# Kernel optimization log

Hardware: AMD Instinct MI355X
Metric: run time of the kernel (lower is better)

Reference implementation:

```python
import jax, jax.numpy as jnp
import numpy as np
from jax import lax

B, C, H, W = 64, 32, 128, 128
E, K = 4, 2
EPS = 1e-5


def setup_inputs() -> dict:
    key = jax.random.key(0)
    ks = jax.random.split(key, 8)
    x = jax.random.normal(ks[0], (B, C, H, W), dtype=jnp.float32)
    weights = jax.random.uniform(ks[1], (B, K), dtype=jnp.float32)
    indices = jax.random.randint(ks[2], (B, K), 0, E, dtype=jnp.int32)
    # stacked per-expert params: conv kernel [E, Co, Ci, 3, 3], BN affine + running stats
    Wc = jax.random.normal(ks[3], (E, C, C, 3, 3), dtype=jnp.float32) * (1.0 / np.sqrt(C * 9))
    gamma = jnp.ones((E, C), dtype=jnp.float32)
    beta = jnp.zeros((E, C), dtype=jnp.float32)
    mean = jax.random.normal(ks[4], (E, C), dtype=jnp.float32) * 0.1
    var = jax.random.uniform(ks[5], (E, C), dtype=jnp.float32) + 0.5
    return {"x": x, "weights": weights, "indices": indices,
            "Wc": Wc, "gamma": gamma, "beta": beta, "mean": mean, "var": var}


def _expert(x, w, g, b, m, v):
    # Conv2d(k=3, s=1, pad=1, no bias) -> BatchNorm2d (inference stats) -> SiLU
    y = lax.conv_general_dilated(x, w, (1, 1), 'SAME',
                                 dimension_numbers=('NCHW', 'OIHW', 'NCHW'))
    scale = (g / jnp.sqrt(v + EPS))[None, :, None, None]
    shift = (b - m * g / jnp.sqrt(v + EPS))[None, :, None, None]
    y = y * scale + shift
    return y * jax.nn.sigmoid(y)  # SiLU


def reference(x, weights, indices, Wc, gamma, beta, mean, var):
    num_experts = Wc.shape[0]
    # combined routing weight per (expert, sample): sum over top-k slots routed to that expert
    onehot = (indices[None, :, :] == jnp.arange(num_experts, dtype=indices.dtype)[:, None, None])  # [E,B,K]
    wcomb = jnp.sum(weights[None, :, :] * onehot.astype(weights.dtype), axis=-1)  # [E,B]
    out = jnp.zeros_like(x)
    for i in range(num_experts):  # small fixed expert count
        y = _expert(x, Wc[i], gamma[i], beta[i], mean[i], var[i])
        out = out + y * wcomb[i][:, None, None, None]
    return out
```

## Files before the change

kernel.cpp:

```cpp
#include <hip/hip_runtime.h>
#include <math.h>


#define B_ 64
#define C_ 32
#define H_ 128
#define W_ 128
#define E_ 4
#define K_ 2
#define EPS_ 1e-5f
#define HW_ (H_ * W_)
#define HP_ 130
#define WP_ 130

#define AROW_B 592
#define A_LDS_B (C_ * AROW_B)
#define XPAD_BYTES ((size_t)B_ * HP_ * WP_ * C_ * 2)
#define AW_OFF   XPAD_BYTES
#define AW_BYTES ((size_t)E_ * A_LDS_B)
#define SCSH_OFF (AW_OFF + AW_BYTES)
#define WS_NEEDED (SCSH_OFF + (size_t)E_ * C_ * 2 * 4)

#define LDS_AW   0
#define LDS_SCSH (2 * A_LDS_B)
#define LDS_TOT  (LDS_SCSH + 512)

typedef __attribute__((ext_vector_type(4))) float  f32x4;
typedef __attribute__((ext_vector_type(8))) short  bf16x8;
typedef __attribute__((ext_vector_type(8))) unsigned short u16x8;
typedef __attribute__((ext_vector_type(4))) unsigned short u16x4;

__device__ inline unsigned short f2bf(float f) {
  unsigned u = __builtin_bit_cast(unsigned, f);
  return (unsigned short)((u + 0x7fffu + ((u >> 16) & 1u)) >> 16);
}

__device__ inline void gload16(const void* g, const void* l) {
  __builtin_amdgcn_global_load_lds(
      (const __attribute__((address_space(1))) unsigned int*)g,
      (__attribute__((address_space(3))) unsigned int*)l, 16, 0, 0);
}

__global__ __launch_bounds__(256, 4)
void prep_kernel(const float* __restrict__ x,
                 const float* __restrict__ Wc,
                 const float* __restrict__ gamma,
                 const float* __restrict__ beta,
                 const float* __restrict__ mean,
                 const float* __restrict__ var,
                 unsigned short* __restrict__ wsu) {
  const int bid = blockIdx.x;
  const int tid = threadIdx.x;

  if (bid >= B_ * HP_) {
    int e = bid - B_ * HP_;
    unsigned short* aw = (unsigned short*)((char*)wsu + AW_OFF) + (size_t)e * (A_LDS_B / 2);
    int co  = tid >> 3;
    int ci4 = (tid & 7) * 4;
    const float* wp = Wc + (((size_t)e * C_ + co) * C_ + ci4) * 9;
    float wv[36];
#pragma unroll
    for (int j = 0; j < 36; ++j) wv[j] = wp[j];
    unsigned short* arow = aw + co * (AROW_B / 2) + ci4;
#pragma unroll
    for (int o = 0; o < 9; ++o) {
      u16x4 pk;
#pragma unroll
      for (int q = 0; q < 4; ++q) pk[q] = f2bf(wv[q * 9 + o]);
      *(u16x4*)(arow + o * C_) = pk;
    }
    if (tid < C_) {
      float g  = gamma[e * C_ + tid];
      float bt = beta[e * C_ + tid];
      float mn = mean[e * C_ + tid];
      float vr = var[e * C_ + tid];
      float sc = g * rsqrtf(vr + EPS_);
      float* scsh = (float*)((char*)wsu + SCSH_OFF);
      scsh[(e * C_ + tid) * 2 + 0] = sc;
      scsh[(e * C_ + tid) * 2 + 1] = bt - mn * sc;
    }
    return;
  }

  const int xg = bid >> 3;
  const int u  = bid & 7;
  const int b  = (xg / HP_) * 8 + u;
  const int hp = xg % HP_;
  unsigned short* xrow = wsu + ((size_t)b * HP_ + hp) * WP_ * C_;

  if (hp == 0 || hp == HP_ - 1) {
    u16x8 z = (u16x8)0;
    for (int c = tid; c < WP_ * C_ / 8; c += 256) *(u16x8*)(xrow + c * 8) = z;
    return;
  }

  __shared__ float tile[C_ * W_];
  const int h = hp - 1;
#pragma unroll
  for (int p = 0; p < 4; ++p) {
    int n  = p * 1024 + tid * 4;
    int c  = n >> 7;
    int px = n & 127;
    *(f32x4*)(tile + n) =
        *(const f32x4*)(x + (((size_t)b * C_ + c) * H_ + h) * W_ + px);
  }
  __syncthreads();

  const int px = tid >> 1;
  const int c0 = (tid & 1) * 16;
  u16x8 o0, o1;
#pragma unroll
  for (int j = 0; j < 8; ++j) o0[j] = f2bf(tile[(c0 + j) * W_ + px]);
#pragma unroll
  for (int j = 0; j < 8; ++j) o1[j] = f2bf(tile[(c0 + 8 + j) * W_ + px]);
  unsigned short* dst = xrow + (px + 1) * C_ + c0;
  *(u16x8*)dst = o0;
  *(u16x8*)(dst + 8) = o1;

  if (tid < 4) {
    int pxb = (tid >> 1) ? (WP_ - 1) : 0;
    int hf  = tid & 1;
    u16x8 z = (u16x8)0;
    unsigned short* d2 = xrow + pxb * C_ + hf * 16;
    *(u16x8*)d2 = z;
    *(u16x8*)(d2 + 8) = z;
  }
}

__global__ __launch_bounds__(256, 3)
void conv_kernel(const unsigned short* __restrict__ xpad,
                 const unsigned short* __restrict__ aw_all,
                 const float* __restrict__ scsh_all,
                 const float* __restrict__ weights,
                 const int* __restrict__ indices,
                 float* __restrict__ out) {
  __shared__ __align__(16) unsigned char lds[LDS_TOT];
  const int tid  = threadIdx.x;
  const int lane = tid & 63;
  const int wid  = tid >> 6;

  const int bid  = blockIdx.x;
  const int xcd  = bid & 7;
  const int ii   = bid >> 3;
  const int b    = (ii >> 5) * 8 + xcd;
  const int reg_ = ii & 31;
  const int rowg = reg_ >> 2;
  const int cseg = reg_ & 3;
  const int c0   = cseg * 32;

  const int   e0  = indices[b * K_ + 0];
  const int   e1  = indices[b * K_ + 1];
  const float wk0 = weights[b * K_ + 0];
  const float wk1 = weights[b * K_ + 1];
  const bool  dup = (e0 == e1);
  const float wka = dup ? (wk0 + wk1) : wk0;

  {
    const int nA = (dup ? 1 : 2) * 1184;
    for (int base = wid * 64; base < nA; base += 256) {
      int c = base + lane;
      int e = (c < 1184) ? e0 : e1;
      int r = (c < 1184) ? c : c - 1184;
      const unsigned short* src = aw_all + (size_t)e * (A_LDS_B / 2) + r * 8;
      if (c < nA) gload16(src, lds + LDS_AW + base * 16);
    }
  }
  if (tid < 2 * C_) {
    int s  = tid >> 5;
    int co = tid & 31;
    int e  = s ? e1 : e0;
    float* d = (float*)(lds + LDS_SCSH) + (s * C_ + co) * 2;
    d[0] = scsh_all[(e * C_ + co) * 2 + 0];
    d[1] = scsh_all[(e * C_ + co) * 2 + 1];
  }
  __syncthreads();

  const int lx = lane & 15;
  const int sl = lane >> 4;
  const float* scshl = (const float*)(lds + LDS_SCSH);

#pragma unroll
  for (int t = 0; t < 2; ++t) {
    const int r0 = rowg * 16 + t * 8 + wid * 2;

    const unsigned short* base =
        xpad + ((size_t)(b * HP_ + r0) * WP_ + c0 + lx) * C_ + sl * 8;

    auto loadrow = [&](bf16x8* dst, int hr) {
#pragma unroll
      for (int s = 0; s < 6; ++s)
        dst[s] = *(const bf16x8*)(base + ((size_t)hr * WP_ + (s / 3) * 16 + (s % 3)) * C_);
    };

    f32x4 acc[2][4][2];
#pragma unroll
    for (int s = 0; s < 2; ++s)
#pragma unroll
      for (int mt = 0; mt < 4; ++mt)
#pragma unroll
        for (int nc = 0; nc < 2; ++nc) acc[s][mt][nc] = (f32x4){0.f, 0.f, 0.f, 0.f};

    bf16x8 FA[6], FB[6];
    loadrow(FA, 0);
    loadrow(FB, 1);

#pragma unroll
    for (int dy = 0; dy < 3; ++dy) {
      bf16x8 FC[6];
      if (dy < 2) loadrow(FC, dy + 2);

#pragma unroll
      for (int dx = 0; dx < 3; ++dx) {
        const int o = dy * 3 + dx;
        bf16x8 bf0[2], bf1[2];
#pragma unroll
        for (int nc = 0; nc < 2; ++nc)
          bf0[nc] = *(const bf16x8*)(lds + LDS_AW + (nc * 16 + lx) * AROW_B + o * 64 + sl * 16);
        if (!dup) {
#pragma unroll
          for (int nc = 0; nc < 2; ++nc)
            bf1[nc] = *(const bf16x8*)(lds + LDS_AW + A_LDS_B + (nc * 16 + lx) * AROW_B + o * 64 + sl * 16);
        }
#pragma unroll
        for (int j = 0; j < 2; ++j)
#pragma unroll
          for (int m2 = 0; m2 < 2; ++m2) {
            bf16x8 A = j ? FB[m2 * 3 + dx] : FA[m2 * 3 + dx];
#pragma unroll
            for (int nc = 0; nc < 2; ++nc)
              acc[0][j * 2 + m2][nc] =
                  __builtin_amdgcn_mfma_f32_16x16x32_bf16(A, bf0[nc], acc[0][j * 2 + m2][nc], 0, 0, 0);
            if (!dup) {
#pragma unroll
              for (int nc = 0; nc < 2; ++nc)
                acc[1][j * 2 + m2][nc] =
                    __builtin_amdgcn_mfma_f32_16x16x32_bf16(A, bf1[nc], acc[1][j * 2 + m2][nc], 0, 0, 0);
            }
          }
      }
#pragma unroll
      for (int s = 0; s < 6; ++s) { FA[s] = FB[s]; FB[s] = FC[s]; }
    }

    f32x4 res[4][2];
#pragma unroll
    for (int mt = 0; mt < 4; ++mt)
#pragma unroll
      for (int nc = 0; nc < 2; ++nc) res[mt][nc] = (f32x4){0.f, 0.f, 0.f, 0.f};

#pragma unroll
    for (int s = 0; s < 2; ++s) {
      if (s == 1 && dup) break;
      float wk = s ? wk1 : wka;
#pragma unroll
      for (int nc = 0; nc < 2; ++nc) {
        int co = nc * 16 + lx;
        float sc = scshl[(s * C_ + co) * 2 + 0];
        float sh = scshl[(s * C_ + co) * 2 + 1];
#pragma unroll
        for (int mt = 0; mt < 4; ++mt) {
#pragma unroll
          for (int r = 0; r < 4; ++r) {
            float y = acc[s][mt][nc][r] * sc + sh;
            float sig = 1.f / (1.f + __expf(-y));
            res[mt][nc][r] += wk * y * sig;
          }
        }
      }
    }

#pragma unroll
    for (int j = 0; j < 2; ++j)
#pragma unroll
      for (int m2 = 0; m2 < 2; ++m2)
#pragma unroll
        for (int nc = 0; nc < 2; ++nc) {
          int co = nc * 16 + lx;
          float* ob = out + ((size_t)b * C_ + co) * HW_ +
                      (size_t)(r0 + j) * W_ + c0 + m2 * 16 + sl * 4;
          *(f32x4*)ob = res[j * 2 + m2][nc];
        }
  }
}

#define FHALO 18
#define FNPX (FHALO * FHALO)
#define FPX_B 64
#define FIN_LDS_B (FNPX * FPX_B)
#define FSC_OFF (FIN_LDS_B + 2 * A_LDS_B)
#define FLDS_TOTAL (FSC_OFF + 2 * C_ * 8)
#define TH 16
#define TW 16

__global__ __launch_bounds__(256, 2)
void moe_fallback_kernel(const float* __restrict__ x,
                         const float* __restrict__ weights,
                         const int* __restrict__ indices,
                         const float* __restrict__ Wc,
                         const float* __restrict__ gamma,
                         const float* __restrict__ beta,
                         const float* __restrict__ mean,
                         const float* __restrict__ var,
                         float* __restrict__ out) {
  __shared__ __align__(16) unsigned char lds[FLDS_TOTAL];
  unsigned char* in_t = lds;
  unsigned char* aw0  = lds + FIN_LDS_B;
  unsigned char* aw1  = lds + FIN_LDS_B + A_LDS_B;
  float*         scsh = (float*)(lds + FSC_OFF);

  const int tid = threadIdx.x;
  const int tiles_per_row = W_ / TW;
  const int tiles_per_img = (H_ / TH) * tiles_per_row;
  const int b    = blockIdx.x / tiles_per_img;
  const int tile = blockIdx.x % tiles_per_img;
  const int th0  = (tile / tiles_per_row) * TH;
  const int tw0  = (tile % tiles_per_row) * TW;

  const int   e0  = indices[b * K_ + 0];
  const int   e1  = indices[b * K_ + 1];
  const float wk0 = weights[b * K_ + 0];
  const float wk1 = weights[b * K_ + 1];
  const bool  dup = (e0 == e1);
  const float wka = dup ? (wk0 + wk1) : wk0;

  const float* xb = x + (size_t)b * C_ * HW_;
  for (int i = tid; i < FNPX * 4; i += 256) {
    int px = i % FNPX;
    int cb = i / FNPX;
    int hy = px / FHALO, hx = px % FHALO;
    int gh = th0 + hy - 1, gw = tw0 + hx - 1;
    u16x8 pk = (u16x8)0;
    if (gh >= 0 && gh < H_ && gw >= 0 && gw < W_) {
      const float* src = xb + (size_t)(cb * 8) * HW_ + (size_t)gh * W_ + gw;
#pragma unroll
      for (int j = 0; j < 8; ++j) pk[j] = f2bf(src[(size_t)j * HW_]);
    }
    int slot = cb ^ (px & 3);
    *(u16x8*)(in_t + px * FPX_B + slot * 16) = pk;
  }
  {
    int co  = tid >> 3;
    int ci4 = (tid & 7) * 4;
#pragma unroll
    for (int s = 0; s < 2; ++s) {
      int e = s ? e1 : e0;
      const float* wp = Wc + (size_t)e * C_ * C_ * 9 + (size_t)co * C_ * 9 + (size_t)ci4 * 9;
      float wv[36];
#pragma unroll
      for (int j = 0; j < 36; ++j) wv[j] = wp[j];
      unsigned char* arow = (s ? aw1 : aw0) + co * AROW_B + ci4 * 2;
#pragma unroll
      for (int o = 0; o < 9; ++o) {
        u16x4 pk;
#pragma unroll
        for (int q = 0; q < 4; ++q) pk[q] = f2bf(wv[q * 9 + o]);
        *(u16x4*)(arow + o * 64) = pk;
      }
    }
  }
  if (tid < 64) {
    int s  = tid >> 5;
    int co = tid & 31;
    int e  = s ? e1 : e0;
    float g  = gamma[e * C_ + co];
    float bt = beta[e * C_ + co];
    float mn = mean[e * C_ + co];
    float vr = var[e * C_ + co];
    float sc = g * rsqrtf(vr + EPS_);
    scsh[(s * C_ + co) * 2 + 0] = sc;
    scsh[(s * C_ + co) * 2 + 1] = bt - mn * sc;
  }
  __syncthreads();

  const int lane = tid & 63;
  const int w    = tid >> 6;
  const int lx   = lane & 15;
  const int sl   = lane >> 4;

  f32x4 acc[2][2][4];
#pragma unroll
  for (int s = 0; s < 2; ++s)
#pragma unroll
    for (int m = 0; m < 2; ++m)
#pragma unroll
      for (int j = 0; j < 4; ++j) acc[s][m][j] = (f32x4){0.f, 0.f, 0.f, 0.f};

  int dy = 0, dx = 0;
#pragma unroll 1
  for (int o = 0; o < 9; ++o) {
    bf16x8 bf[4];
#pragma unroll
    for (int j = 0; j < 4; ++j) {
      int hp   = (4 * w + j + dy) * FHALO + (lx + dx);
      int slot = sl ^ (hp & 3);
      bf[j] = *(const bf16x8*)(in_t + hp * FPX_B + slot * 16);
    }
    bf16x8 af0[2], af1[2];
#pragma unroll
    for (int m = 0; m < 2; ++m) {
      int ro = (m * 16 + lx) * AROW_B + o * 64 + sl * 16;
      af0[m] = *(const bf16x8*)(aw0 + ro);
      af1[m] = *(const bf16x8*)(aw1 + ro);
    }
#pragma unroll
    for (int m = 0; m < 2; ++m)
#pragma unroll
      for (int j = 0; j < 4; ++j)
        acc[0][m][j] = __builtin_amdgcn_mfma_f32_16x16x32_bf16(af0[m], bf[j], acc[0][m][j], 0, 0, 0);
    if (!dup) {
#pragma unroll
      for (int m = 0; m < 2; ++m)
#pragma unroll
        for (int j = 0; j < 4; ++j)
          acc[1][m][j] = __builtin_amdgcn_mfma_f32_16x16x32_bf16(af1[m], bf[j], acc[1][m][j], 0, 0, 0);
    }
    if (++dx == 3) { dx = 0; ++dy; }
  }

  float res[2][4][4];
#pragma unroll
  for (int m = 0; m < 2; ++m)
#pragma unroll
    for (int j = 0; j < 4; ++j)
#pragma unroll
      for (int r = 0; r < 4; ++r) res[m][j][r] = 0.f;

#pragma unroll
  for (int s = 0; s < 2; ++s) {
    if (s == 1 && dup) break;
    float wk = s ? wk1 : wka;
#pragma unroll
    for (int m = 0; m < 2; ++m)
#pragma unroll
      for (int r = 0; r < 4; ++r) {
        int co = m * 16 + sl * 4 + r;
        float sc = scsh[(s * C_ + co) * 2 + 0];
        float sh = scsh[(s * C_ + co) * 2 + 1];
#pragma unroll
        for (int j = 0; j < 4; ++j) {
          float y = acc[s][m][j][r] * sc + sh;
          float sig = 1.f / (1.f + __expf(-y));
          res[m][j][r] += wk * y * sig;
        }
      }
  }
#pragma unroll
  for (int m = 0; m < 2; ++m)
#pragma unroll
    for (int r = 0; r < 4; ++r) {
      int co = m * 16 + sl * 4 + r;
      float* ob = out + ((size_t)b * C_ + co) * HW_ + (size_t)th0 * W_ + tw0 + lx;
#pragma unroll
      for (int j = 0; j < 4; ++j)
        ob[(size_t)(4 * w + j) * W_] = res[m][j][r];
    }
}

extern "C" void kernel_launch(void* const* d_in, const int* in_sizes, int n_in,
                              void* d_out, int out_size, void* d_ws, size_t ws_size,
                              hipStream_t stream) {
  const float* x       = (const float*)d_in[0];
  const float* weights = (const float*)d_in[1];
  const int*   indices = (const int*)d_in[2];
  const float* Wc      = (const float*)d_in[3];
  const float* gamma   = (const float*)d_in[4];
  const float* beta    = (const float*)d_in[5];
  const float* mean    = (const float*)d_in[6];
  const float* var     = (const float*)d_in[7];
  float* out = (float*)d_out;

  if (d_ws != nullptr && ws_size >= WS_NEEDED) {
    unsigned short* wsu = (unsigned short*)d_ws;
    const unsigned short* aw_all   = (const unsigned short*)((char*)d_ws + AW_OFF);
    const float*          scsh_all = (const float*)((char*)d_ws + SCSH_OFF);
    prep_kernel<<<B_ * HP_ + E_, 256, 0, stream>>>(x, Wc, gamma, beta, mean, var, wsu);
    conv_kernel<<<2048, 256, 0, stream>>>(wsu, aw_all, scsh_all, weights, indices, out);
  } else {
    moe_fallback_kernel<<<B_ * 64, 256, 0, stream>>>(
        x, weights, indices, Wc, gamma, beta, mean, var, out);
  }
}
```

Measured before the change: 103.7 us.

## Halve conv grid, process 4 row-tiles per block with prefetch and MFMA priority

```diff
diff --git a/kernel.cpp b/kernel.cpp
--- a/kernel.cpp
+++ b/kernel.cpp
@@ -142,8 +142,8 @@
   const int bid  = blockIdx.x;
   const int xcd  = bid & 7;
   const int ii   = bid >> 3;
-  const int b    = (ii >> 5) * 8 + xcd;
-  const int reg_ = ii & 31;
+  const int b    = (ii >> 4) * 8 + xcd;
+  const int reg_ = ii & 15;
   const int rowg = reg_ >> 2;
   const int cseg = reg_ & 3;
   const int c0   = cseg * 32;
@@ -173,24 +173,33 @@
     d[0] = scsh_all[(e * C_ + co) * 2 + 0];
     d[1] = scsh_all[(e * C_ + co) * 2 + 1];
   }
-  __syncthreads();
 
   const int lx = lane & 15;
   const int sl = lane >> 4;
+
+  const unsigned short* cbase =
+      xpad + ((size_t)b * HP_ * WP_ + c0 + lx) * C_ + sl * 8;
+
+#define LOADROW(dst, rbase, hr)                                              \
+  {                                                                          \
+    const unsigned short* _p = cbase + ((size_t)((rbase) + (hr)) * WP_) * C_; \
+    _Pragma("unroll")                                                        \
+    for (int s_ = 0; s_ < 6; ++s_)                                           \
+      dst[s_] = *(const bf16x8*)(_p + ((s_ / 3) * 16 + (s_ % 3)) * C_);      \
+  }
+
+  bf16x8 FA[6], FB[6];
+  const int r0base0 = rowg * 32 + wid * 2;
+  LOADROW(FA, r0base0, 0)
+  LOADROW(FB, r0base0, 1)
+
+  __syncthreads();
+
   const float* scshl = (const float*)(lds + LDS_SCSH);
 
-#pragma unroll
-  for (int t = 0; t < 2; ++t) {
-    const int r0 = rowg * 16 + t * 8 + wid * 2;
-
-    const unsigned short* base =
-        xpad + ((size_t)(b * HP_ + r0) * WP_ + c0 + lx) * C_ + sl * 8;
-
-    auto loadrow = [&](bf16x8* dst, int hr) {
-#pragma unroll
-      for (int s = 0; s < 6; ++s)
-        dst[s] = *(const bf16x8*)(base + ((size_t)hr * WP_ + (s / 3) * 16 + (s % 3)) * C_);
-    };
+#pragma unroll 1
+  for (int t = 0; t < 4; ++t) {
+    const int r0 = rowg * 32 + t * 8 + wid * 2;
 
     f32x4 acc[2][4][2];
 #pragma unroll
@@ -199,15 +208,11 @@
       for (int mt = 0; mt < 4; ++mt)
 #pragma unroll
         for (int nc = 0; nc < 2; ++nc) acc[s][mt][nc] = (f32x4){0.f, 0.f, 0.f, 0.f};
-
-    bf16x8 FA[6], FB[6];
-    loadrow(FA, 0);
-    loadrow(FB, 1);
 
 #pragma unroll
     for (int dy = 0; dy < 3; ++dy) {
       bf16x8 FC[6];
-      if (dy < 2) loadrow(FC, dy + 2);
+      if (dy < 2) LOADROW(FC, r0, dy + 2)
 
 #pragma unroll
       for (int dx = 0; dx < 3; ++dx) {
@@ -221,6 +226,7 @@
           for (int nc = 0; nc < 2; ++nc)
             bf1[nc] = *(const bf16x8*)(lds + LDS_AW + A_LDS_B + (nc * 16 + lx) * AROW_B + o * 64 + sl * 16);
         }
+        __builtin_amdgcn_s_setprio(1);
 #pragma unroll
         for (int j = 0; j < 2; ++j)
 #pragma unroll
@@ -237,9 +243,16 @@
                     __builtin_amdgcn_mfma_f32_16x16x32_bf16(A, bf1[nc], acc[1][j * 2 + m2][nc], 0, 0, 0);
             }
           }
+        __builtin_amdgcn_s_setprio(0);
       }
 #pragma unroll
       for (int s = 0; s < 6; ++s) { FA[s] = FB[s]; FB[s] = FC[s]; }
+    }
+
+    if (t < 3) {
+      const int rn = r0 + 8;
+      LOADROW(FA, rn, 0)
+      LOADROW(FB, rn, 1)
     }
 
     f32x4 res[4][2];
@@ -474,7 +487,7 @@
     const unsigned short* aw_all   = (const unsigned short*)((char*)d_ws + AW_OFF);
     const float*          scsh_all = (const float*)((char*)d_ws + SCSH_OFF);
     prep_kernel<<<B_ * HP_ + E_, 256, 0, stream>>>(x, Wc, gamma, beta, mean, var, wsu);
-    conv_kernel<<<2048, 256, 0, stream>>>(wsu, aw_all, scsh_all, weights, indices, out);
+    conv_kernel<<<1024, 256, 0, stream>>>(wsu, aw_all, scsh_all, weights, indices, out);
   } else {
     moe_fallback_kernel<<<B_ * 64, 256, 0, stream>>>(
         x, weights, indices, Wc, gamma, beta, mean, var, out);
```

New measurement: 207.6 us. 100% more time.
